# Kernel tuning notes

Hardware: AMD Instinct MI355X
Metric: run time of the kernel (lower is better)

Reference implementation:

```python
import jax, jax.numpy as jnp
import numpy as np

H, N2, R = 512, 16, 32   # hidden_dim, state_dim//2, dt_rank=ceil(512/16)
B, L = 1, 4096


def setup_inputs() -> dict:
    key = jax.random.key(0)
    ks = jax.random.split(key, 7)
    u = jax.random.normal(ks[0], (B, L, H), dtype=jnp.float32)
    # Parameter initialization mirroring S4DKernel.__init__
    A_log = jnp.zeros((H, N2), jnp.float32)                      # log(ones)
    A_im = jnp.broadcast_to(jnp.arange(N2, dtype=jnp.float32), (H, N2)).copy()
    B_param = jax.random.normal(ks[1], (H, N2, 2), jnp.float32)
    C_param = jax.random.normal(ks[2], (H, N2, 2), jnp.float32)
    D = jax.random.normal(ks[3], (H,), jnp.float32)
    dt_w = jax.random.normal(ks[4], (H, R), jnp.float32) / np.sqrt(R)
    dt_min, dt_max, dt_floor = 1e-3, 0.1, 1e-4
    dt_init = jnp.exp(jax.random.uniform(ks[5], (H,), jnp.float32)
                      * (np.log(dt_max) - np.log(dt_floor)) + np.log(dt_floor))
    dt_init = jnp.maximum(dt_init, dt_min)
    dt_b = dt_init + jnp.log(-jnp.expm1(-dt_init))               # inverse-softplus init
    xproj_w = jax.random.normal(ks[6], (R, H), jnp.float32) / np.sqrt(H)
    return {"u": u, "A_log": A_log, "A_im": A_im, "B_param": B_param,
            "C_param": C_param, "D": D, "dt_w": dt_w, "dt_b": dt_b,
            "xproj_w": xproj_w}


def reference(u, A_log, A_im, B_param, C_param, D, dt_w, dt_b, xproj_w):
    # Complex continuous-time parameters
    A = -jnp.exp(A_log) + 1j * A_im                 # [H, N2]
    Bc = B_param[..., 0] + 1j * B_param[..., 1]     # [H, N2]
    Cc = C_param[..., 0] + 1j * C_param[..., 1]     # [H, N2]

    # dt path: x_proj_for_dt (no bias) -> dt_proj -> softplus
    dt_u = jnp.einsum('blh,rh->blr', u, xproj_w)                    # [B,L,R]
    dt = jax.nn.softplus(jnp.einsum('blr,hr->blh', dt_u, dt_w) + dt_b)  # [B,L,H]

    # ZOH discretization
    z = dt[..., None] * A                           # [B,L,H,N2] complex
    A_bar = jnp.exp(z)
    B_bar_div = jnp.where(jnp.abs(z) < 1e-4, 1.0 + z / 2, (jnp.exp(z) - 1.0) / z)
    ub = u[..., None].astype(A_bar.dtype) * B_bar_div * Bc          # [B,L,H,N2]

    # Parallel scan for h_k = A_k * h_{k-1} + u_k (first-order linear recurrence)
    def op(c1, c2):
        a1, b1 = c1
        a2, b2 = c2
        return a1 * a2, a2 * b1 + b2
    _, h = jax.lax.associative_scan(op, (A_bar, ub), axis=1)        # [B,L,H,N2]

    y = jnp.einsum('blhn,hn->blh', h, Cc) + u * D
    return y.real
```

## Files before the change

### kernel.cpp

```cpp
#include <hip/hip_runtime.h>

#define Hd 512
#define N2d 16
#define Rd 32
#define Ld 4096
#define NCHUNK 128
#define CLEN (Ld / NCHUNK)
#define NCH (Hd * N2d)
#define NGRP 16
#define NGROUPS (NCHUNK / NGRP)


__global__ __launch_bounds__(256) void k_dt(const float* __restrict__ u,
                                            const float* __restrict__ xproj_w,
                                            const float* __restrict__ dt_w,
                                            const float* __restrict__ dt_b,
                                            float2* __restrict__ du_out) {
    __shared__ float u_s[8][Hd];
    __shared__ float dtu_s[8][Rd];
    const int t = threadIdx.x;
    const int l0 = blockIdx.x * 8;
    const int cch = l0 >> 5;
    const int lp  = l0 & 31;

    #pragma unroll
    for (int i = 0; i < 16; ++i) {
        int idx = t + i * 256;
        ((float*)u_s)[idx] = u[l0 * Hd + idx];
    }
    __syncthreads();

    const int r = t >> 3;
    const int j = t & 7;
    float part[8];
    #pragma unroll
    for (int l = 0; l < 8; ++l) part[l] = 0.f;
    for (int k = 0; k < 64; ++k) {
        float w = xproj_w[r * Hd + k * 8 + j];
        #pragma unroll
        for (int l = 0; l < 8; ++l) part[l] = fmaf(u_s[l][k * 8 + j], w, part[l]);
    }
    #pragma unroll
    for (int off = 1; off < 8; off <<= 1) {
        #pragma unroll
        for (int l = 0; l < 8; ++l) part[l] += __shfl_xor(part[l], off);
    }
    if (j == 0) {
        #pragma unroll
        for (int l = 0; l < 8; ++l) dtu_s[l][r] = part[l];
    }
    __syncthreads();

    #pragma unroll
    for (int hb = 0; hb < 2; ++hb) {
        int h = hb * 256 + t;
        float bias = dt_b[h];
        float acc[8];
        #pragma unroll
        for (int l = 0; l < 8; ++l) acc[l] = bias;
        #pragma unroll
        for (int rb = 0; rb < 8; ++rb) {
            float4 w = *(const float4*)&dt_w[h * Rd + rb * 4];
            #pragma unroll
            for (int l = 0; l < 8; ++l) {
                acc[l] = fmaf(dtu_s[l][rb * 4 + 0], w.x, acc[l]);
                acc[l] = fmaf(dtu_s[l][rb * 4 + 1], w.y, acc[l]);
                acc[l] = fmaf(dtu_s[l][rb * 4 + 2], w.z, acc[l]);
                acc[l] = fmaf(dtu_s[l][rb * 4 + 3], w.w, acc[l]);
            }
        }
        float2 vals[8];
        #pragma unroll
        for (int l = 0; l < 8; ++l) {
            float x = acc[l];
            float sp = fmaxf(x, 0.f) + log1pf(__expf(-fabsf(x)));
            float uv = u_s[l][h];
            float us = uv * __builtin_amdgcn_rcpf(fmaxf(sp, 1e-30f));
            vals[l] = make_float2(sp, us);
        }
        float4* d4 = (float4*)&du_out[((size_t)cch * Hd + h) * CLEN + lp];
        #pragma unroll
        for (int i = 0; i < 4; ++i)
            d4[i] = make_float4(vals[2 * i].x, vals[2 * i].y,
                                vals[2 * i + 1].x, vals[2 * i + 1].y);
    }
}

__global__ __launch_bounds__(256) void k_chunk(const float2* __restrict__ du,
        const float* __restrict__ A_log, const float* __restrict__ A_im,
        const float* __restrict__ B_param, const float* __restrict__ C_param,
        const float* __restrict__ Dp,
        float2* __restrict__ Sb, float* __restrict__ Tc,
        float2* __restrict__ y1T) {
    const int t = threadIdx.x;
    const int q = t & 3;
    const int hh = blockIdx.y * 64 + (t >> 2);
    const int c = blockIdx.x;
    const int hnb = hh * N2d + q * 4;

    const float2* rowb = du + ((size_t)c * Hd + hh) * CLEN;
    float2* y1row = y1T + ((size_t)c * Hd + hh) * CLEN;

    float alog[4], Aim[4];
    #pragma unroll
    for (int j = 0; j < 4; ++j) {
        alog[j] = A_log[hnb + j];
        Aim[j] = A_im[hnb + j];
    }
    float d1 = Aim[1] - Aim[0], d2 = Aim[2] - Aim[1], d3 = Aim[3] - Aim[2];
    const bool fast = (alog[1] == alog[0]) && (alog[2] == alog[0]) &&
                      (alog[3] == alog[0]) && (d1 == d2) && (d2 == d3);
    float Are[4];
    if (fast) {
        Are[0] = -__expf(alog[0]);
        Are[1] = Are[2] = Are[3] = Are[0];
    } else {
        #pragma unroll
        for (int j = 0; j < 4; ++j) Are[j] = -__expf(alog[j]);
    }
    float BAr[4], BAi[4], Cre[4], Cim[4];
    #pragma unroll
    for (int j = 0; j < 4; ++j) {
        int hn = hnb + j;
        float Bre = B_param[2 * hn];
        float Bim = B_param[2 * hn + 1];
        float inv = __builtin_amdgcn_rcpf(Are[j] * Are[j] + Aim[j] * Aim[j]);
        BAr[j] = (Bre * Are[j] + Bim * Aim[j]) * inv;
        BAi[j] = (Bim * Are[j] - Bre * Aim[j]) * inv;
        Cre[j] = C_param[2 * hn];
        Cim[j] = C_param[2 * hn + 1];
    }
    const float Dv = Dp[hh];

    float sr[4] = {0.f, 0.f, 0.f, 0.f}, si[4] = {0.f, 0.f, 0.f, 0.f};
    float sdt = 0.f;

    float2 b0[8], b1[8];

    #define LOADB(buf, bb)                                                     \
        { const float4* r4 = (const float4*)(rowb + (bb) * 8);                 \
          _Pragma("unroll")                                                    \
          for (int k4 = 0; k4 < 4; ++k4) {                                     \
              float4 v = r4[k4];                                               \
              buf[2 * k4]     = make_float2(v.x, v.y);                         \
              buf[2 * k4 + 1] = make_float2(v.z, v.w);                         \
          } }

    #define YWRITE(bb)                                                         \
        if (q == 0) {                                                          \
            float4* y4 = (float4*)(y1row + (bb) * 8);                          \
            _Pragma("unroll")                                                  \
            for (int i = 0; i < 4; ++i)                                        \
                y4[i] = make_float4(yb[2 * i].x, yb[2 * i].y,                  \
                                    yb[2 * i + 1].x, yb[2 * i + 1].y);         \
        }

    if (fast) {
        const float Are0 = Are[0], Aim0 = Aim[0], dA = Aim[1] - Aim[0];
        #define STEPF(buf, bb)                                                 \
            { float2 yb[8];                                                    \
              _Pragma("unroll")                                                \
              for (int k = 0; k < 8; ++k) {                                    \
                float dtv = buf[k].x, us = buf[k].y;                           \
                sdt += dtv;                                                    \
                float er = __expf(dtv * Are0);                                 \
                float s0, c0, sd, cd;                                          \
                __sincosf(dtv * Aim0, &s0, &c0);                               \
                __sincosf(dtv * dA, &sd, &cd);                                 \
                float ar = er * c0, ai = er * s0;                              \
                float yv = 0.f;                                                \
                _Pragma("unroll")                                              \
                for (int jj = 0; jj < 4; ++jj) {                               \
                    float gr = fmaf(ar, us, -us);                              \
                    float gi = ai * us;                                        \
                    float nr = fmaf(ar, sr[jj], fmaf(-ai, si[jj],              \
                                 fmaf(gr, BAr[jj], -gi * BAi[jj])));           \
                    float ni = fmaf(ar, si[jj], fmaf( ai, sr[jj],              \
                                 fmaf(gr, BAi[jj],  gi * BAr[jj])));           \
                    sr[jj] = nr; si[jj] = ni;                                  \
                    yv = fmaf(nr, Cre[jj], fmaf(-ni, Cim[jj], yv));            \
                    if (jj < 3) {                                              \
                        float tr = fmaf(ar, cd, -ai * sd);                     \
                        ai = fmaf(ai, cd, ar * sd);                            \
                        ar = tr;                                               \
                    }                                                          \
                }                                                              \
                yv += __shfl_xor(yv, 1);                                       \
                yv += __shfl_xor(yv, 2);                                       \
                yb[k] = make_float2(fmaf(dtv * us, Dv, yv), sdt);              \
              }                                                                \
              YWRITE(bb) }
        LOADB(b0, 0);
        LOADB(b1, 1); STEPF(b0, 0);
        LOADB(b0, 2); STEPF(b1, 1);
        LOADB(b1, 3); STEPF(b0, 2);
        STEPF(b1, 3);
        #undef STEPF
    } else {
        #define STEPS(buf, bb)                                                 \
            { float2 yb[8];                                                    \
              _Pragma("unroll")                                                \
              for (int k = 0; k < 8; ++k) {                                    \
                float dtv = buf[k].x, us = buf[k].y;                           \
                sdt += dtv;                                                    \
                float yv = 0.f;                                                \
                _Pragma("unroll")                                              \
                for (int jj = 0; jj < 4; ++jj) {                               \
                    float er = __expf(dtv * Are[jj]);                          \
                    float s, cc;                                               \
                    __sincosf(dtv * Aim[jj], &s, &cc);                         \
                    float ar = er * cc, ai = er * s;                           \
                    float gr = fmaf(ar, us, -us);                              \
                    float gi = ai * us;                                        \
                    float nr = fmaf(ar, sr[jj], fmaf(-ai, si[jj],              \
                                 fmaf(gr, BAr[jj], -gi * BAi[jj])));           \
                    float ni = fmaf(ar, si[jj], fmaf( ai, sr[jj],              \
                                 fmaf(gr, BAi[jj],  gi * BAr[jj])));           \
                    sr[jj] = nr; si[jj] = ni;                                  \
                    yv = fmaf(nr, Cre[jj], fmaf(-ni, Cim[jj], yv));            \
                }                                                              \
                yv += __shfl_xor(yv, 1);                                       \
                yv += __shfl_xor(yv, 2);                                       \
                yb[k] = make_float2(fmaf(dtv * us, Dv, yv), sdt);              \
              }                                                                \
              YWRITE(bb) }
        LOADB(b0, 0);
        LOADB(b1, 1); STEPS(b0, 0);
        LOADB(b0, 2); STEPS(b1, 1);
        LOADB(b1, 3); STEPS(b0, 2);
        STEPS(b1, 3);
        #undef STEPS
    }
    #undef LOADB
    #undef YWRITE

    int base = c * NCH + hnb;
    #pragma unroll
    for (int jj = 0; jj < 4; ++jj)
        Sb[base + jj] = make_float2(sr[jj], si[jj]);
    if (q == 0) Tc[hh * NCHUNK + c] = sdt;
}

__global__ __launch_bounds__(256) void k_comb(const float2* __restrict__ Sb,
        const float* __restrict__ Tc, const float* __restrict__ A_log,
        const float* __restrict__ A_im, const float* __restrict__ C_param,
        float2* __restrict__ W) {
    __shared__ float4 agg_s[32][NGROUPS + 1];
    __shared__ float Tc_s[2][NCHUNK];
    const int t = threadIdx.x;
    const int g = t >> 5;
    const int cl = t & 31;
    const int chain = blockIdx.x * 32 + cl;
    const int h0 = blockIdx.x * 2;

    {
        int cc = t & 127;
        int hs = t >> 7;
        Tc_s[hs][cc] = Tc[(h0 + hs) * NCHUNK + cc];
    }
    __syncthreads();

    const int hsel = cl >> 4;
    const float Are = -__expf(A_log[chain]);
    const float Aim = A_im[chain];

    float2 s[NGRP];
    float pr[NGRP], pi[NGRP];
    #pragma unroll
    for (int i = 0; i < NGRP; ++i) {
        int c = g * NGRP + i;
        s[i] = Sb[c * NCH + chain];
        float T = Tc_s[hsel][c];
        float er = __expf(Are * T);
        float sn, cs;
        __sincosf(Aim * T, &sn, &cs);
        pr[i] = er * cs;
        pi[i] = er * sn;
    }

    float Pr = 1.f, Pi = 0.f, Hr = 0.f, Hi = 0.f;
    #pragma unroll
    for (int i = 0; i < NGRP; ++i) {
        float nhr = fmaf(pr[i], Hr, fmaf(-pi[i], Hi, s[i].x));
        float nhi = fmaf(pr[i], Hi, fmaf( pi[i], Hr, s[i].y));
        float npr = fmaf(pr[i], Pr, -pi[i] * Pi);
        float npi = fmaf(pr[i], Pi,  pi[i] * Pr);
        Hr = nhr; Hi = nhi; Pr = npr; Pi = npi;
    }
    agg_s[cl][g] = make_float4(Pr, Pi, Hr, Hi);
    __syncthreads();

    float hr = 0.f, hi = 0.f;
    for (int j = 0; j < g; ++j) {
        float4 a = agg_s[cl][j];
        float nr = fmaf(a.x, hr, fmaf(-a.y, hi, a.z));
        float ni = fmaf(a.x, hi, fmaf( a.y, hr, a.w));
        hr = nr; hi = ni;
    }

    const float Cr = C_param[2 * chain];
    const float Ci = C_param[2 * chain + 1];
    #pragma unroll
    for (int i = 0; i < NGRP; ++i) {
        int c = g * NGRP + i;
        W[c * NCH + chain] = make_float2(fmaf(Cr, hr, -Ci * hi),
                                         fmaf(Cr, hi,  Ci * hr));
        float nr = fmaf(pr[i], hr, fmaf(-pi[i], hi, s[i].x));
        float ni = fmaf(pr[i], hi, fmaf( pi[i], hr, s[i].y));
        hr = nr; hi = ni;
    }
}

__global__ __launch_bounds__(256) void k_corr(const float2* __restrict__ y1T,
        const float* __restrict__ A_log, const float* __restrict__ A_im,
        const float2* __restrict__ W, float* __restrict__ out) {
    const int t = threadIdx.x;
    const int c = blockIdx.x;
    const int hl = t & 63;
    const int h = blockIdx.y * 64 + hl;
    const int lb = t >> 6;
    const int l0 = c * CLEN + lb * 8;
    const int hn0 = h * N2d;

    float2 yt[8];
    {
        const float4* y4 = (const float4*)(y1T + ((size_t)c * Hd + h) * CLEN + lb * 8);
        #pragma unroll
        for (int i = 0; i < 4; ++i) {
            float4 v = y4[i];
            yt[2 * i]     = make_float2(v.x, v.y);
            yt[2 * i + 1] = make_float2(v.z, v.w);
        }
    }

    float2 w[N2d];
    {
        const float4* w4 = reinterpret_cast<const float4*>(&W[c * NCH + hn0]);
        #pragma unroll
        for (int n = 0; n < 8; ++n) {
            float4 v = w4[n];
            w[2 * n]     = make_float2(v.x, v.y);
            w[2 * n + 1] = make_float2(v.z, v.w);
        }
    }

    float alog[N2d], aim[N2d];
    #pragma unroll
    for (int n = 0; n < N2d; ++n) {
        alog[n] = A_log[hn0 + n];
        aim[n] = A_im[hn0 + n];
    }
    float dA = aim[1] - aim[0];
    bool fast = true;
    #pragma unroll
    for (int n = 1; n < N2d; ++n)
        fast = fast && (alog[n] == alog[0]) && (aim[n] - aim[n - 1] == dA);

    if (fast) {
        const float Are0 = -__expf(alog[0]);
        const float Aim0 = aim[0];
        #pragma unroll
        for (int k = 0; k < 8; ++k) {
            float T = yt[k].y;
            float er = __expf(Are0 * T);
            float s0, c0, sd, cd;
            __sincosf(Aim0 * T, &s0, &c0);
            __sincosf(dA * T, &sd, &cd);
            float ar = er * c0, ai = er * s0;
            float corr = 0.f;
            #pragma unroll
            for (int n = 0; n < N2d; ++n) {
                corr = fmaf(ar, w[n].x, fmaf(-ai, w[n].y, corr));
                if (n < N2d - 1) {
                    float tr = fmaf(ar, cd, -ai * sd);
                    ai = fmaf(ai, cd, ar * sd);
                    ar = tr;
                }
            }
            out[(l0 + k) * Hd + h] = yt[k].x + corr;
        }
    } else {
        float are[N2d];
        #pragma unroll
        for (int n = 0; n < N2d; ++n) are[n] = -__expf(alog[n]);
        #pragma unroll
        for (int k = 0; k < 8; ++k) {
            float T = yt[k].y;
            float corr = 0.f;
            #pragma unroll
            for (int n = 0; n < N2d; ++n) {
                float er = __expf(are[n] * T);
                float s, cc;
                __sincosf(aim[n] * T, &s, &cc);
                corr = fmaf(er * cc, w[n].x, fmaf(-er * s, w[n].y, corr));
            }
            out[(l0 + k) * Hd + h] = yt[k].x + corr;
        }
    }
}

extern "C" void kernel_launch(void* const* d_in, const int* in_sizes, int n_in,
                              void* d_out, int out_size, void* d_ws, size_t ws_size,
                              hipStream_t stream) {
    const float* u        = (const float*)d_in[0];
    const float* A_log    = (const float*)d_in[1];
    const float* A_im     = (const float*)d_in[2];
    const float* B_param  = (const float*)d_in[3];
    const float* C_param  = (const float*)d_in[4];
    const float* Dp       = (const float*)d_in[5];
    const float* dt_w     = (const float*)d_in[6];
    const float* dt_b     = (const float*)d_in[7];
    const float* xproj_w  = (const float*)d_in[8];

    float2* du  = (float2*)d_ws;
    float2* Sb  = du + (size_t)Ld * Hd;
    float2* W   = Sb + (size_t)NCHUNK * NCH;
    float2* y1T = W + (size_t)NCHUNK * NCH;
    float*  Tc  = (float*)(y1T + (size_t)Ld * Hd);
    float*  out = (float*)d_out;

    k_dt<<<Ld / 8, 256, 0, stream>>>(u, xproj_w, dt_w, dt_b, du);
    dim3 g2(NCHUNK, Hd / 64);
    k_chunk<<<g2, 256, 0, stream>>>(du, A_log, A_im, B_param, C_param, Dp,
                                    Sb, Tc, y1T);
    k_comb<<<NCH / 32, 256, 0, stream>>>(Sb, Tc, A_log, A_im, C_param, W);
    k_corr<<<g2, 256, 0, stream>>>(y1T, A_log, A_im, W, out);
}
```

Baseline: 132.4 us.

## Fuse dt projection and softplus into chunk scan kernel via shared memory

The second half of the dt computation (dt_w projection, softplus, u/dt) moves from the first kernel into the chunk kernel. The first kernel now writes only the small rank-32 dt_u array. The chunk kernel loads u and dt_u tiles into shared memory, computes dt and u/dt per chunk, and reads them from LDS instead of a global float2 buffer. This removes the round trip of the L×H float2 intermediate through global memory. In exchange it adds shared memory use, an extra barrier phase, and redundant loads of dt_w per block.

```diff
diff --git a/kernel.cpp b/kernel.cpp
--- a/kernel.cpp
+++ b/kernel.cpp
@@ -11,17 +11,12 @@
 #define NGROUPS (NCHUNK / NGRP)
 
 
-__global__ __launch_bounds__(256) void k_dt(const float* __restrict__ u,
-                                            const float* __restrict__ xproj_w,
-                                            const float* __restrict__ dt_w,
-                                            const float* __restrict__ dt_b,
-                                            float2* __restrict__ du_out) {
+__global__ __launch_bounds__(256) void k_dtu(const float* __restrict__ u,
+                                             const float* __restrict__ xproj_w,
+                                             float* __restrict__ dtu) {
     __shared__ float u_s[8][Hd];
-    __shared__ float dtu_s[8][Rd];
     const int t = threadIdx.x;
     const int l0 = blockIdx.x * 8;
-    const int cch = l0 >> 5;
-    const int lp  = l0 & 31;
 
     #pragma unroll
     for (int i = 0; i < 16; ++i) {
@@ -47,58 +42,78 @@
     }
     if (j == 0) {
         #pragma unroll
-        for (int l = 0; l < 8; ++l) dtu_s[l][r] = part[l];
-    }
-    __syncthreads();
-
-    #pragma unroll
-    for (int hb = 0; hb < 2; ++hb) {
-        int h = hb * 256 + t;
-        float bias = dt_b[h];
-        float acc[8];
-        #pragma unroll
-        for (int l = 0; l < 8; ++l) acc[l] = bias;
-        #pragma unroll
-        for (int rb = 0; rb < 8; ++rb) {
-            float4 w = *(const float4*)&dt_w[h * Rd + rb * 4];
-            #pragma unroll
-            for (int l = 0; l < 8; ++l) {
-                acc[l] = fmaf(dtu_s[l][rb * 4 + 0], w.x, acc[l]);
-                acc[l] = fmaf(dtu_s[l][rb * 4 + 1], w.y, acc[l]);
-                acc[l] = fmaf(dtu_s[l][rb * 4 + 2], w.z, acc[l]);
-                acc[l] = fmaf(dtu_s[l][rb * 4 + 3], w.w, acc[l]);
-            }
-        }
-        float2 vals[8];
-        #pragma unroll
-        for (int l = 0; l < 8; ++l) {
-            float x = acc[l];
-            float sp = fmaxf(x, 0.f) + log1pf(__expf(-fabsf(x)));
-            float uv = u_s[l][h];
-            float us = uv * __builtin_amdgcn_rcpf(fmaxf(sp, 1e-30f));
-            vals[l] = make_float2(sp, us);
-        }
-        float4* d4 = (float4*)&du_out[((size_t)cch * Hd + h) * CLEN + lp];
-        #pragma unroll
-        for (int i = 0; i < 4; ++i)
-            d4[i] = make_float4(vals[2 * i].x, vals[2 * i].y,
-                                vals[2 * i + 1].x, vals[2 * i + 1].y);
+        for (int l = 0; l < 8; ++l) dtu[(l0 + l) * Rd + r] = part[l];
     }
 }
 
-__global__ __launch_bounds__(256) void k_chunk(const float2* __restrict__ du,
+__global__ __launch_bounds__(256) void k_chunk(const float* __restrict__ u,
+        const float* __restrict__ dtu, const float* __restrict__ dt_w,
+        const float* __restrict__ dt_b,
         const float* __restrict__ A_log, const float* __restrict__ A_im,
         const float* __restrict__ B_param, const float* __restrict__ C_param,
         const float* __restrict__ Dp,
         float2* __restrict__ Sb, float* __restrict__ Tc,
         float2* __restrict__ y1T) {
+    __shared__ float u_s[CLEN][64];
+    __shared__ float dtu_s[CLEN][Rd];
+    __shared__ float2 du_s[CLEN][64];
     const int t = threadIdx.x;
+    const int c = blockIdx.x;
+    const int hg = blockIdx.y;
+
+    {
+        const float* ub = u + (size_t)(c * CLEN) * Hd + hg * 64;
+        #pragma unroll
+        for (int i = 0; i < 2; ++i) {
+            int idx = i * 256 + t;
+            int row = idx >> 4;
+            int col = idx & 15;
+            *(float4*)&u_s[row][col * 4] = *(const float4*)(ub + (size_t)row * Hd + col * 4);
+        }
+    }
+    {
+        const float4* db = (const float4*)(dtu + (size_t)c * CLEN * Rd);
+        *(((float4*)dtu_s) + t) = db[t];
+    }
+    __syncthreads();
+
+    {
+        const int hl2 = t & 63;
+        const int h = hg * 64 + hl2;
+        const int lb2 = t >> 6;
+        const float bias = dt_b[h];
+        const float4* w4 = (const float4*)&dt_w[h * Rd];
+        float acc[8];
+        #pragma unroll
+        for (int k = 0; k < 8; ++k) acc[k] = bias;
+        #pragma unroll
+        for (int rb = 0; rb < 8; ++rb) {
+            float4 w = w4[rb];
+            #pragma unroll
+            for (int k = 0; k < 8; ++k) {
+                int l = lb2 * 8 + k;
+                acc[k] = fmaf(dtu_s[l][rb * 4 + 0], w.x, acc[k]);
+                acc[k] = fmaf(dtu_s[l][rb * 4 + 1], w.y, acc[k]);
+                acc[k] = fmaf(dtu_s[l][rb * 4 + 2], w.z, acc[k]);
+                acc[k] = fmaf(dtu_s[l][rb * 4 + 3], w.w, acc[k]);
+            }
+        }
+        #pragma unroll
+        for (int k = 0; k < 8; ++k) {
+            int l = lb2 * 8 + k;
+            float x = acc[k];
+            float sp = fmaxf(x, 0.f) + log1pf(__expf(-fabsf(x)));
+            float uv = u_s[l][hl2];
+            float us = uv * __builtin_amdgcn_rcpf(fmaxf(sp, 1e-30f));
+            du_s[l][hl2] = make_float2(sp, us);
+        }
+    }
+    __syncthreads();
+
     const int q = t & 3;
-    const int hh = blockIdx.y * 64 + (t >> 2);
-    const int c = blockIdx.x;
+    const int hl = t >> 2;
+    const int hh = hg * 64 + hl;
     const int hnb = hh * N2d + q * 4;
-
-    const float2* rowb = du + ((size_t)c * Hd + hh) * CLEN;
     float2* y1row = y1T + ((size_t)c * Hd + hh) * CLEN;
 
     float alog[4], Aim[4];
@@ -135,17 +150,6 @@
     float sr[4] = {0.f, 0.f, 0.f, 0.f}, si[4] = {0.f, 0.f, 0.f, 0.f};
     float sdt = 0.f;
 
-    float2 b0[8], b1[8];
-
-    #define LOADB(buf, bb)                                                     \
-        { const float4* r4 = (const float4*)(rowb + (bb) * 8);                 \
-          _Pragma("unroll")                                                    \
-          for (int k4 = 0; k4 < 4; ++k4) {                                     \
-              float4 v = r4[k4];                                               \
-              buf[2 * k4]     = make_float2(v.x, v.y);                         \
-              buf[2 * k4 + 1] = make_float2(v.z, v.w);                         \
-          } }
-
     #define YWRITE(bb)                                                         \
         if (q == 0) {                                                          \
             float4* y4 = (float4*)(y1row + (bb) * 8);                          \
@@ -157,81 +161,74 @@
 
     if (fast) {
         const float Are0 = Are[0], Aim0 = Aim[0], dA = Aim[1] - Aim[0];
-        #define STEPF(buf, bb)                                                 \
-            { float2 yb[8];                                                    \
-              _Pragma("unroll")                                                \
-              for (int k = 0; k < 8; ++k) {                                    \
-                float dtv = buf[k].x, us = buf[k].y;                           \
-                sdt += dtv;                                                    \
-                float er = __expf(dtv * Are0);                                 \
-                float s0, c0, sd, cd;                                          \
-                __sincosf(dtv * Aim0, &s0, &c0);                               \
-                __sincosf(dtv * dA, &sd, &cd);                                 \
-                float ar = er * c0, ai = er * s0;                              \
-                float yv = 0.f;                                                \
-                _Pragma("unroll")                                              \
-                for (int jj = 0; jj < 4; ++jj) {                               \
-                    float gr = fmaf(ar, us, -us);                              \
-                    float gi = ai * us;                                        \
-                    float nr = fmaf(ar, sr[jj], fmaf(-ai, si[jj],              \
-                                 fmaf(gr, BAr[jj], -gi * BAi[jj])));           \
-                    float ni = fmaf(ar, si[jj], fmaf( ai, sr[jj],              \
-                                 fmaf(gr, BAi[jj],  gi * BAr[jj])));           \
-                    sr[jj] = nr; si[jj] = ni;                                  \
-                    yv = fmaf(nr, Cre[jj], fmaf(-ni, Cim[jj], yv));            \
-                    if (jj < 3) {                                              \
-                        float tr = fmaf(ar, cd, -ai * sd);                     \
-                        ai = fmaf(ai, cd, ar * sd);                            \
-                        ar = tr;                                               \
-                    }                                                          \
-                }                                                              \
-                yv += __shfl_xor(yv, 1);                                       \
-                yv += __shfl_xor(yv, 2);                                       \
-                yb[k] = make_float2(fmaf(dtv * us, Dv, yv), sdt);              \
-              }                                                                \
-              YWRITE(bb) }
-        LOADB(b0, 0);
-        LOADB(b1, 1); STEPF(b0, 0);
-        LOADB(b0, 2); STEPF(b1, 1);
-        LOADB(b1, 3); STEPF(b0, 2);
-        STEPF(b1, 3);
-        #undef STEPF
+        #pragma unroll
+        for (int bb = 0; bb < 4; ++bb) {
+            float2 yb[8];
+            #pragma unroll
+            for (int k = 0; k < 8; ++k) {
+                float2 d = du_s[bb * 8 + k][hl];
+                float dtv = d.x, us = d.y;
+                sdt += dtv;
+                float er = __expf(dtv * Are0);
+                float s0, c0, sd, cd;
+                __sincosf(dtv * Aim0, &s0, &c0);
+                __sincosf(dtv * dA, &sd, &cd);
+                float ar = er * c0, ai = er * s0;
+                float yv = 0.f;
+                #pragma unroll
+                for (int jj = 0; jj < 4; ++jj) {
+                    float gr = fmaf(ar, us, -us);
+                    float gi = ai * us;
+                    float nr = fmaf(ar, sr[jj], fmaf(-ai, si[jj],
+                                 fmaf(gr, BAr[jj], -gi * BAi[jj])));
+                    float ni = fmaf(ar, si[jj], fmaf( ai, sr[jj],
+                                 fmaf(gr, BAi[jj],  gi * BAr[jj])));
+                    sr[jj] = nr; si[jj] = ni;
+                    yv = fmaf(nr, Cre[jj], fmaf(-ni, Cim[jj], yv));
+                    if (jj < 3) {
+                        float tr = fmaf(ar, cd, -ai * sd);
+                        ai = fmaf(ai, cd, ar * sd);
+                        ar = tr;
+                    }
+                }
+                yv += __shfl_xor(yv, 1);
+                yv += __shfl_xor(yv, 2);
+                yb[k] = make_float2(fmaf(dtv * us, Dv, yv), sdt);
+            }
+            YWRITE(bb)
+        }
     } else {
-        #define STEPS(buf, bb)                                                 \
-            { float2 yb[8];                                                    \
-              _Pragma("unroll")                                                \
-              for (int k = 0; k < 8; ++k) {                                    \
-                float dtv = buf[k].x, us = buf[k].y;                           \
-                sdt += dtv;                                                    \
-                float yv = 0.f;                                                \
-                _Pragma("unroll")                                              \
-                for (int jj = 0; jj < 4; ++jj) {                               \
-                    float er = __expf(dtv * Are[jj]);                          \
-                    float s, cc;                                               \
-                    __sincosf(dtv * Aim[jj], &s, &cc);                         \
-                    float ar = er * cc, ai = er * s;                           \
-                    float gr = fmaf(ar, us, -us);                              \
-                    float gi = ai * us;                                        \
-                    float nr = fmaf(ar, sr[jj], fmaf(-ai, si[jj],              \
-                                 fmaf(gr, BAr[jj], -gi * BAi[jj])));           \
-                    float ni = fmaf(ar, si[jj], fmaf( ai, sr[jj],              \
-                                 fmaf(gr, BAi[jj],  gi * BAr[jj])));           \
-                    sr[jj] = nr; si[jj] = ni;                                  \
-                    yv = fmaf(nr, Cre[jj], fmaf(-ni, Cim[jj], yv));            \
-                }                                                              \
-                yv += __shfl_xor(yv, 1);                                       \
-                yv += __shfl_xor(yv, 2);                                       \
-                yb[k] = make_float2(fmaf(dtv * us, Dv, yv), sdt);              \
-              }                                                                \
-              YWRITE(bb) }
-        LOADB(b0, 0);
-        LOADB(b1, 1); STEPS(b0, 0);
-        LOADB(b0, 2); STEPS(b1, 1);
-        LOADB(b1, 3); STEPS(b0, 2);
-        STEPS(b1, 3);
-        #undef STEPS
-    }
-    #undef LOADB
+        #pragma unroll
+        for (int bb = 0; bb < 4; ++bb) {
+            float2 yb[8];
+            #pragma unroll
+            for (int k = 0; k < 8; ++k) {
+                float2 d = du_s[bb * 8 + k][hl];
+                float dtv = d.x, us = d.y;
+                sdt += dtv;
+                float yv = 0.f;
+                #pragma unroll
+                for (int jj = 0; jj < 4; ++jj) {
+                    float er = __expf(dtv * Are[jj]);
+                    float s, cc;
+                    __sincosf(dtv * Aim[jj], &s, &cc);
+                    float ar = er * cc, ai = er * s;
+                    float gr = fmaf(ar, us, -us);
+                    float gi = ai * us;
+                    float nr = fmaf(ar, sr[jj], fmaf(-ai, si[jj],
+                                 fmaf(gr, BAr[jj], -gi * BAi[jj])));
+                    float ni = fmaf(ar, si[jj], fmaf( ai, sr[jj],
+                                 fmaf(gr, BAi[jj],  gi * BAr[jj])));
+                    sr[jj] = nr; si[jj] = ni;
+                    yv = fmaf(nr, Cre[jj], fmaf(-ni, Cim[jj], yv));
+                }
+                yv += __shfl_xor(yv, 1);
+                yv += __shfl_xor(yv, 2);
+                yb[k] = make_float2(fmaf(dtv * us, Dv, yv), sdt);
+            }
+            YWRITE(bb)
+        }
+    }
     #undef YWRITE
 
     int base = c * NCH + hnb;
@@ -412,17 +409,17 @@
     const float* dt_b     = (const float*)d_in[7];
     const float* xproj_w  = (const float*)d_in[8];
 
-    float2* du  = (float2*)d_ws;
-    float2* Sb  = du + (size_t)Ld * Hd;
+    float*  dtu = (float*)d_ws;
+    float2* Sb  = (float2*)(dtu + (size_t)Ld * Rd);
     float2* W   = Sb + (size_t)NCHUNK * NCH;
     float2* y1T = W + (size_t)NCHUNK * NCH;
     float*  Tc  = (float*)(y1T + (size_t)Ld * Hd);
     float*  out = (float*)d_out;
 
-    k_dt<<<Ld / 8, 256, 0, stream>>>(u, xproj_w, dt_w, dt_b, du);
+    k_dtu<<<Ld / 8, 256, 0, stream>>>(u, xproj_w, dtu);
     dim3 g2(NCHUNK, Hd / 64);
-    k_chunk<<<g2, 256, 0, stream>>>(du, A_log, A_im, B_param, C_param, Dp,
-                                    Sb, Tc, y1T);
+    k_chunk<<<g2, 256, 0, stream>>>(u, dtu, dt_w, dt_b, A_log, A_im,
+                                    B_param, C_param, Dp, Sb, Tc, y1T);
     k_comb<<<NCH / 32, 256, 0, stream>>>(Sb, Tc, A_log, A_im, C_param, W);
     k_corr<<<g2, 256, 0, stream>>>(y1T, A_log, A_im, W, out);
 }
```

After: 128.0 us. 3.3% less time.
